# Kernel tuning notes

Measured on AMD Instinct MI355X. Metric: run time of the kernel, lower is better.

## Reference

```python
import jax, jax.numpy as jnp
import numpy as np

ALPHA = 0.1       # args.alpha
T = 1.0           # args.T temperature
SIGMA = 64.0      # Gaussian kernel bandwidth of kernel_function
B_CONST = 1.0     # B in get_lambda
N_ITERS = 50      # 2^-50 << tol=1e-8, matches the break condition of the 1000-iter loop
HW = 256          # image resolution (upsample target)


def _features(feat):
    # get_feature: bilinear upsample (align_corners=False == half-pixel, as jax.image.resize) then sigmoid(x/T)
    n, c, _, _ = feat.shape
    up = jax.image.resize(feat, (n, c, HW, HW), method='bilinear')
    return jax.nn.sigmoid(up / T)


def setup_inputs() -> dict:
    key = jax.random.key(0)
    k1, k2, k3, k4 = jax.random.split(key, 4)
    return {
        'cal_feat': jax.random.normal(k1, (256, 1, 64, 64), jnp.float32),
        'test_feat': jax.random.normal(k2, (32, 1, 64, 64), jnp.float32),
        'cal_gt': jax.random.randint(k3, (256, 1, 256, 256), 0, 2, jnp.int32),
        'test_gt': jax.random.randint(k4, (32, 1, 256, 256), 0, 2, jnp.int32),
    }


def reference(cal_feat, test_feat, cal_gt, test_gt):
    cal_res = _features(cal_feat)    # [N,1,H,W] in (0,1)
    test_res = _features(test_feat)  # [B,1,H,W]
    N = cal_res.shape[0]
    B = test_res.shape[0]
    f32 = cal_res.dtype

    # kernel_function.get_weight: Gaussian RBF on flattened features, plus self-weight 1, row-normalized -> [B, N+1]
    cf = cal_res.reshape(N, -1)
    tf = test_res.reshape(B, -1)
    d2 = (tf * tf).sum(-1)[:, None] + (cf * cf).sum(-1)[None, :] - 2.0 * (tf @ cf.T)
    k = jnp.exp(-d2 / (2.0 * SIGMA * SIGMA))
    w = jnp.concatenate([k, jnp.ones((B, 1), f32)], axis=1)
    w = w / w.sum(axis=1, keepdims=True)

    # FNR_i(t) = #{positive pixels of cal sample i with score < t} / #positives
    # (pred = res >= t, so false negatives are positive pixels with res < t). Precompute sorted
    # positive-pixel scores per cal sample so the bisection is a batched searchsorted.
    gt = (cal_gt > 0).reshape(N, -1)
    pos = jnp.sum(gt, axis=1)                                    # [N]
    scores = jnp.where(gt, cal_res.reshape(N, -1), jnp.inf)
    sorted_scores = jnp.sort(scores, axis=1)                     # [N, HW*HW], padding at +inf
    pos_f = jnp.maximum(pos, 1).astype(f32)

    def fnr_at(t):  # t: [B] thresholds -> [N, B]
        cnt = jax.vmap(lambda s: jnp.searchsorted(s, t, side='left'))(sorted_scores)
        return cnt.astype(f32) / pos_f[:, None]

    # batched bisection on lambda (get_lambda, vectorized over the B test samples)
    def body(carry, _):
        low, high = carry
        lam = 0.5 * (low + high)
        fnr = fnr_at(1.0 - lam)                                   # [N, B]
        risk = jnp.einsum('bn,nb->b', w[:, :-1], fnr) + w[:, -1] * B_CONST
        high = jnp.where(risk < ALPHA, lam, high)
        low = jnp.where(risk >= ALPHA, lam, low)
        return (low, high), None

    init = (jnp.zeros((B,), f32), jnp.ones((B,), f32))
    (low, _), _ = jax.lax.scan(body, init, None, length=N_ITERS)
    lam = low  # _lambda = low after the loop

    # prediction set, size and per-test FNR (get_fnr_list on the test sample)
    pred = test_res >= (1.0 - lam)[:, None, None, None]           # [B,1,H,W] bool
    size = jnp.sum(pred, axis=(1, 2, 3)).astype(f32)
    tgt = test_gt > 0
    tp = jnp.sum(pred & tgt, axis=(1, 2, 3)).astype(f32)
    tpos = jnp.maximum(jnp.sum(tgt, axis=(1, 2, 3)), 1).astype(f32)
    fnr_test = 1.0 - tp / tpos                                    # fdr_tensor, [B]
    return fnr_test, lam, size
```

## Files before the change

kernel.cpp:

```cpp
#include <hip/hip_runtime.h>


#define NPIX 65536
#define HB 16256
#define CDF_STRIDE 16272
#define ALPHA 0.1f
#define STAGE_CAP 35840

#define OFF_TESTRES  0
#define OFF_CALBF    8388608u
#define OFF_TESTBF   41943040u
#define OFF_GROUPED  46137344u
#define OFF_CDF      79691776u
#define OFF_GPART    88023040u
#define OFF_CC       90120192u
#define OFF_THR      90121216u
#define OFF_LAM      90121344u
#define OFF_FACC     90121472u
#define OFF_CDFT     90122240u

typedef __attribute__((ext_vector_type(8))) short bf16x8;
typedef __attribute__((ext_vector_type(16))) float f32x16;

__device__ __forceinline__ unsigned short f2bf_rne(float f) {
  unsigned u = __float_as_uint(f);
  return (unsigned short)((u + 0x7FFFu + ((u >> 16) & 1u)) >> 16);
}

__device__ __forceinline__ int SW(int w) { return w ^ ((w >> 5) & 31); }

__device__ __forceinline__ float sig_v(float a, float b, float wy) {
  float v = a * (1.f - wy) + b * wy;
  return 1.f / (1.f + __expf(-v));
}

__global__ __launch_bounds__(1024, 2) void k_calt(const float* __restrict__ featc,
                                                  const int* __restrict__ gt,
                                                  unsigned short* __restrict__ calbf,
                                                  unsigned short* __restrict__ cdf,
                                                  unsigned short* __restrict__ grouped,
                                                  float* __restrict__ cc,
                                                  const float* __restrict__ featt,
                                                  float* __restrict__ tres,
                                                  unsigned short* __restrict__ tbf) {
  __shared__ unsigned smem[17313];
  __shared__ float sfeat[4096];
  __shared__ __align__(16) unsigned short sstage[STAGE_CAP];
  float* tfeat = (float*)sstage;
  unsigned* gmask = (unsigned*)(sstage + 8192);
  const int tid = threadIdx.x;
  const int lane = tid & 63, wv = tid >> 6;
  const int x = tid & 255, yq = tid >> 8;
  float sx = 0.25f * (float)x - 0.375f;
  int x0 = (int)floorf(sx);
  float wx = sx - (float)x0;
  int x1 = x0 + 1;
  if (x0 < 0) x0 = 0;
  if (x1 > 63) x1 = 63;

  const int n = blockIdx.x;
  const int b = n >> 3, sl = n & 7;
  for (int i = tid; i < HB; i += 1024) smem[i] = 0;
  for (int i = tid; i < 4096; i += 1024) {
    sfeat[i] = featc[n * 4096 + i];
    tfeat[i] = featt[b * 4096 + i];
  }
  {
    const int4* gt4 = (const int4*)(gt + (size_t)n * NPIX);
    for (int w = tid; w < 2048; w += 1024) {
      unsigned m = 0;
      #pragma unroll
      for (int j = 0; j < 8; ++j) {
        int4 g = gt4[w * 8 + j];
        m |= (g.x > 0 ? 1u : 0u) << (j * 4);
        m |= (g.y > 0 ? 2u : 0u) << (j * 4);
        m |= (g.z > 0 ? 4u : 0u) << (j * 4);
        m |= (g.w > 0 ? 8u : 0u) << (j * 4);
      }
      gmask[w] = m;
    }
  }
  unsigned short* cbn = calbf + (size_t)n * NPIX;
  __syncthreads();

  {
    const float* tf0 = tfeat + x0;
    const float* tf1 = tfeat + x1;
    float* resb = tres + (size_t)b * NPIX;
    unsigned short* tbn = tbf + (size_t)b * NPIX;
    const int mt0 = sl * 8 + yq * 2;
    int rp = mt0 - 1 < 0 ? 0 : mt0 - 1;
    float hp = tf0[rp * 64] * (1.f - wx) + tf1[rp * 64] * wx;
    float hc = tf0[mt0 * 64] * (1.f - wx) + tf1[mt0 * 64] * wx;
    #pragma unroll
    for (int q = 0; q < 2; ++q) {
      int m = mt0 + q;
      int rn = m + 1 > 63 ? 63 : m + 1;
      float hn = tf0[rn * 64] * (1.f - wx) + tf1[rn * 64] * wx;
      #pragma unroll
      for (int j = 0; j < 4; ++j) {
        int y = 4 * m + j;
        float sy = 0.25f * (float)y - 0.375f;
        int y0 = (int)floorf(sy);
        float wy = sy - (float)y0;
        float s = sig_v(j < 2 ? hp : hc, j < 2 ? hc : hn, wy);
        int p = (y << 8) + x;
        resb[p] = s;
        tbn[p] = f2bf_rne(s);
      }
      hp = hc; hc = hn;
    }
  }

  const float* f0 = sfeat + x0;
  const float* f1 = sfeat + x1;
  const int m0 = yq * 16;
  unsigned long long pm = 0ull;
  float sumsq = 0.f;
  {
    int rp = m0 - 1 < 0 ? 0 : m0 - 1;
    float hp = f0[rp * 64] * (1.f - wx) + f1[rp * 64] * wx;
    float hc = f0[m0 * 64] * (1.f - wx) + f1[m0 * 64] * wx;
    #pragma unroll 4
    for (int q = 0; q < 16; ++q) {
      int m = m0 + q;
      int rn = m + 1 > 63 ? 63 : m + 1;
      float hn = f0[rn * 64] * (1.f - wx) + f1[rn * 64] * wx;
      #pragma unroll
      for (int j = 0; j < 4; ++j) {
        int y = 4 * m + j;
        float sy = 0.25f * (float)y - 0.375f;
        int y0 = (int)floorf(sy);
        float wy = sy - (float)y0;
        float s = sig_v(j < 2 ? hp : hc, j < 2 ? hc : hn, wy);
        int p = (y << 8) + x;
        unsigned short bh = f2bf_rne(s);
        cbn[p] = bh;
        float sr = __uint_as_float((unsigned)bh << 16);
        sumsq += sr * sr;
        if ((gmask[p >> 5] >> (x & 31)) & 1u) {
          pm |= (1ull << (q * 4 + j));
          atomicAdd(&smem[SW((int)(__float_as_uint(s) >> 16))], 1u);
        }
      }
      hp = hc; hc = hn;
    }
  }
  #pragma unroll
  for (int off = 32; off; off >>= 1) sumsq += __shfl_xor(sumsq, off);
  if (lane == 0) smem[16272 + wv] = __float_as_uint(sumsq);
  __syncthreads();
  if (tid == 0) {
    float c = 0.f;
    for (int w = 0; w < 16; ++w) c += __uint_as_float(smem[16272 + w]);
    cc[n] = c;
  }
  const int base = tid * 16;
  unsigned psum = 0;
  if (tid < 1016) {
    #pragma unroll
    for (int j = 0; j < 16; ++j) psum += smem[SW(base + j)];
  }
  unsigned inc = psum;
  #pragma unroll
  for (int off = 1; off < 64; off <<= 1) {
    unsigned v = __shfl_up(inc, off);
    if (lane >= off) inc += v;
  }
  if (lane == 63) smem[16256 + wv] = inc;
  smem[16288 + tid] = inc - psum;
  __syncthreads();
  {
    unsigned woff = 0;
    for (int w = 0; w < wv; ++w) woff += smem[16256 + w];
    unsigned run = woff + smem[16288 + tid];
    if (tid < 1016) {
      #pragma unroll
      for (int j = 0; j < 16; ++j) {
        int si = SW(base + j);
        unsigned h = smem[si];
        smem[si] = run;
        run += h;
      }
    }
    if (tid == 1015) smem[17312] = run;
  }
  __syncthreads();
  unsigned short* cdfn = cdf + (size_t)n * CDF_STRIDE;
  for (int i = tid; i < HB; i += 1024) cdfn[i] = (unsigned short)smem[SW(i)];
  const unsigned pos = smem[17312];
  if (tid == 0) cdfn[HB] = (unsigned short)pos;
  __syncthreads();
  unsigned short* gn = grouped + (size_t)n * NPIX;
  {
    int rp = m0 - 1 < 0 ? 0 : m0 - 1;
    float hp = f0[rp * 64] * (1.f - wx) + f1[rp * 64] * wx;
    float hc = f0[m0 * 64] * (1.f - wx) + f1[m0 * 64] * wx;
    for (int q = 0; q < 16; ++q) {
      int m = m0 + q;
      int rn = m + 1 > 63 ? 63 : m + 1;
      float hn = f0[rn * 64] * (1.f - wx) + f1[rn * 64] * wx;
      unsigned nib = (unsigned)(pm >> (q * 4)) & 0xFu;
      if (nib) {
        #pragma unroll
        for (int j = 0; j < 4; ++j) {
          if (nib & (1u << j)) {
            int y = 4 * m + j;
            float sy = 0.25f * (float)y - 0.375f;
            int y0 = (int)floorf(sy);
            float wy = sy - (float)y0;
            float s = sig_v(j < 2 ? hp : hc, j < 2 ? hc : hn, wy);
            unsigned bits = __float_as_uint(s);
            unsigned idx = atomicAdd(&smem[SW((int)(bits >> 16))], 1u);
            unsigned short lo = (unsigned short)(bits & 0xFFFFu);
            if (idx < STAGE_CAP) sstage[idx] = lo;
            else gn[idx] = lo;
          }
        }
      }
      hp = hc; hc = hn;
    }
  }
  __syncthreads();
  unsigned lim = pos < STAGE_CAP ? pos : STAGE_CAP;
  for (unsigned i = tid; i < lim; i += 1024) gn[i] = sstage[i];
}

__global__ __launch_bounds__(256) void k_tr(const unsigned short* __restrict__ cdf,
                                            unsigned short* __restrict__ cdfT) {
  __shared__ unsigned short tile[256][136];
  const int b0 = blockIdx.x * 128;
  const int tid = threadIdx.x;
  const unsigned short* src = cdf + (size_t)tid * CDF_STRIDE + b0;
  #pragma unroll
  for (int j = 0; j < 128; j += 8)
    *(int4*)&tile[tid][j] = *(const int4*)(src + j);
  __syncthreads();
  for (int j = 0; j < 128; ++j)
    cdfT[(size_t)(b0 + j) * 256 + tid] = tile[tid][j];
}

__global__ __launch_bounds__(256) void k_gemm(const unsigned short* __restrict__ tbf,
                                              const unsigned short* __restrict__ cbf,
                                              float* __restrict__ gpart) {
  __shared__ __align__(16) unsigned short As[16384];
  __shared__ __align__(16) unsigned short Bs[16384];
  __shared__ float lred[4][1024];
  const int tid = threadIdx.x;
  const int lane = tid & 63, wv = tid >> 6;
  const int r = lane & 31, half = lane >> 5;
  const int nt = blockIdx.x;
  f32x16 acc;
  #pragma unroll
  for (int i = 0; i < 16; ++i) acc[i] = 0.f;
  for (int ch = 0; ch < 2; ++ch) {
    const size_t kbase = (size_t)blockIdx.y * 1024 + ch * 512;
    __syncthreads();
    #pragma unroll
    for (int s = 0; s < 16; ++s) {
      int flat = s * 256 + tid;
      int rem = flat & 2047;
      int row = rem >> 6, kb = rem & 63;
      const unsigned short* src = (flat >= 2048)
          ? cbf + (size_t)(nt * 32 + row) * NPIX + kbase + kb * 8
          : tbf + (size_t)row * NPIX + kbase + kb * 8;
      int slot = ((kb << 5) + row) ^ (kb & 31);
      int4 v = *(const int4*)src;
      *(int4*)((flat >= 2048 ? Bs : As) + slot * 8) = v;
    }
    __syncthreads();
    #pragma unroll
    for (int i = 0; i < 8; ++i) {
      int k8 = (wv << 4) + i * 2 + half;
      int slot = ((k8 << 5) + r) ^ (k8 & 31);
      bf16x8 a = *(const bf16x8*)(As + slot * 8);
      bf16x8 b = *(const bf16x8*)(Bs + slot * 8);
      acc = __builtin_amdgcn_mfma_f32_32x32x16_bf16(a, b, acc, 0, 0, 0);
    }
  }
  #pragma unroll
  for (int rg = 0; rg < 16; ++rg) {
    int m = (rg & 3) + 8 * (rg >> 2) + 4 * half;
    lred[wv][m * 32 + r] = acc[rg];
  }
  __syncthreads();
  float* gp = gpart + (size_t)(blockIdx.y * 8 + nt) * 1024;
  for (int e = tid; e < 1024; e += 256)
    gp[e] = lred[0][e] + lred[1][e] + lred[2][e] + lred[3][e];
}

__global__ __launch_bounds__(512) void k_quantw(const float* __restrict__ gpart,
                                                const float* __restrict__ cc,
                                                const unsigned short* __restrict__ tbf,
                                                const unsigned short* __restrict__ cdf,
                                                const unsigned short* __restrict__ cdfT,
                                                const unsigned short* __restrict__ grouped,
                                                float* __restrict__ lam,
                                                float* __restrict__ thr,
                                                int* __restrict__ facc) {
  __shared__ float qs[256];
  __shared__ float bins[4096];
  __shared__ float red[8];
  __shared__ float tpart[16];
  __shared__ float bc[3];
  __shared__ unsigned sBin;
  const int b = blockIdx.x, tid = threadIdx.x;
  const int lane = tid & 63, wv = tid >> 6;

  if (tid < 4) facc[b * 4 + tid] = 0;
  for (int i = tid; i < 4096; i += 512) bins[i] = 0.f;
  if (tid == 0) sBin = 0xFFFFFFFFu;

  {
    const unsigned short* tbn = tbf + (size_t)b * NPIX;
    const int xa = tid & 255, ya = tid >> 8;
    const int yb = ya + 2;
    float sa = 0.f, sb = 0.f;
    #pragma unroll 4
    for (int it = 0; it < 64; ++it) {
      float ra = __uint_as_float((unsigned)tbn[((it * 4 + ya) << 8) + xa] << 16);
      float rb = __uint_as_float((unsigned)tbn[((it * 4 + yb) << 8) + xa] << 16);
      sa += ra * ra;
      sb += rb * rb;
    }
    #pragma unroll
    for (int off = 32; off; off >>= 1) {
      sa += __shfl_xor(sa, off);
      sb += __shfl_xor(sb, off);
    }
    if (lane == 0) { tpart[wv] = sa; tpart[8 + wv] = sb; }
  }
  __syncthreads();
  if (tid == 0) {
    float t = 0.f;
    for (int w = 0; w < 16; ++w) t += tpart[w];
    bc[2] = t;
  }
  float g = 0.f;
  if (tid < 256) {
    const float* gp = gpart + ((tid >> 5) * 1024) + (b * 32) + (tid & 31);
    #pragma unroll 8
    for (int ks = 0; ks < 64; ++ks) g += gp[(size_t)ks * 8192];
  }
  __syncthreads();
  float k = 0.f;
  if (tid < 256) {
    float d2 = bc[2] + cc[tid] - 2.f * g;
    k = expf(-d2 * (1.f / 8192.f));
  }
  float v = k;
  #pragma unroll
  for (int off = 32; off; off >>= 1) v += __shfl_xor(v, off);
  if (lane == 0) red[wv] = v;
  __syncthreads();
  if (tid == 0) {
    float ws = 1.f;
    for (int w = 0; w < 8; ++w) ws += red[w];
    bc[0] = ws;
  }
  __syncthreads();
  const float wsum = bc[0];
  const float wlast = 1.f / wsum;
  const float R = ALPHA - wlast;
  if (R <= 0.f) {
    if (tid == 0) { lam[b] = 1.0f; thr[b] = 0.0f; }
    return;
  }
  if (tid < 256) {
    unsigned pos = cdf[(size_t)tid * CDF_STRIDE + HB];
    qs[tid] = k / (wsum * (float)(pos ? pos : 1u));
  }
  __syncthreads();

  int lo = 0, hi = HB;
  float baseS = 0.f;
  for (int it = 0; it < 14; ++it) {
    int mid = (lo + hi) >> 1;
    float p = 0.f;
    if (tid < 256) p = qs[tid] * (float)cdfT[(size_t)mid * 256 + tid];
    float r = p;
    #pragma unroll
    for (int off = 32; off; off >>= 1) r += __shfl_xor(r, off);
    if (lane == 0) red[wv] = r;
    __syncthreads();
    if (tid == 0) {
      float s = 0.f;
      for (int w = 0; w < 8; ++w) s += red[w];
      bc[1] = s;
    }
    __syncthreads();
    float S = bc[1];
    if (S < R) { lo = mid; baseS = S; } else { hi = mid; }
  }
  const int B = lo;

  {
    const int n = tid >> 1;
    const float q = qs[n];
    const unsigned short* cn = cdf + (size_t)n * CDF_STRIDE;
    const unsigned short* gn = grouped + (size_t)n * NPIX;
    unsigned e0 = cn[B + 1];
    for (unsigned j = (unsigned)cn[B] + (tid & 1); j < e0; j += 2)
      atomicAdd(&bins[gn[j] >> 4], q);
  }
  __syncthreads();

  if (wv == 0) {
    float s = 0.f;
    for (int j = 0; j < 64; ++j) s += bins[lane * 64 + j];
    float inc = s;
    #pragma unroll
    for (int off = 1; off < 64; off <<= 1) {
      float u = __shfl_up(inc, off);
      if (lane >= off) inc += u;
    }
    float pre = inc - s;
    bool hit = (baseS + pre < R) && (baseS + inc >= R);
    unsigned long long m = __ballot(hit);
    int ow = m ? (__ffsll((unsigned long long)m) - 1) : -1;
    if (lane == ow) {
      float run = baseS + pre;
      unsigned bin = (unsigned)lane * 64 + 63;
      for (int j = 0; j < 64; ++j) {
        float bv = bins[lane * 64 + j];
        if (run + bv >= R) { bin = (unsigned)lane * 64 + j; break; }
        run += bv;
      }
      sBin = bin;
    }
    if (m == 0 && lane == 0) sBin = 4095u;
  }
  __syncthreads();
  if (tid == 0) {
    unsigned tb = ((unsigned)B << 16) | (sBin << 4);
    lam[b] = 1.0f - __uint_as_float(tb | 0x8u);
    thr[b] = __uint_as_float((tb | 0xFu) + 1u);
  }
}

__global__ __launch_bounds__(256) void k_finalp(const float* __restrict__ tres,
                                                const int* __restrict__ tgt,
                                                const float* __restrict__ thr,
                                                const float* __restrict__ lam,
                                                int* __restrict__ facc,
                                                float* __restrict__ out) {
  __shared__ int red[12];
  const int b = blockIdx.x, seg = blockIdx.y, tid = threadIdx.x;
  const int lane = tid & 63, wv = tid >> 6;
  const float th = thr[b];
  const float4* rb4 = (const float4*)(tres + (size_t)b * NPIX + seg * 8192);
  const int4* gb4 = (const int4*)(tgt + (size_t)b * NPIX + seg * 8192);
  int sz = 0, tp = 0, tpos = 0;
  #pragma unroll
  for (int i = 0; i < 8; ++i) {
    float4 r4 = rb4[i * 256 + tid];
    int4 g4 = gb4[i * 256 + tid];
    int p0 = (r4.x >= th), t0 = (g4.x > 0);
    int p1 = (r4.y >= th), t1 = (g4.y > 0);
    int p2 = (r4.z >= th), t2 = (g4.z > 0);
    int p3 = (r4.w >= th), t3 = (g4.w > 0);
    sz += p0 + p1 + p2 + p3;
    tp += (p0 & t0) + (p1 & t1) + (p2 & t2) + (p3 & t3);
    tpos += t0 + t1 + t2 + t3;
  }
  #pragma unroll
  for (int off = 32; off; off >>= 1) {
    sz += __shfl_xor(sz, off);
    tp += __shfl_xor(tp, off);
    tpos += __shfl_xor(tpos, off);
  }
  if (lane == 0) { red[wv] = sz; red[4 + wv] = tp; red[8 + wv] = tpos; }
  __syncthreads();
  if (tid == 0) {
    int s0 = red[0] + red[1] + red[2] + red[3];
    int s1 = red[4] + red[5] + red[6] + red[7];
    int s2 = red[8] + red[9] + red[10] + red[11];
    atomicAdd(&facc[b * 4 + 0], s0);
    atomicAdd(&facc[b * 4 + 1], s1);
    atomicAdd(&facc[b * 4 + 2], s2);
    __threadfence();
    int done = atomicAdd(&facc[b * 4 + 3], 1);
    if (done == 7) {
      int f0 = atomicAdd(&facc[b * 4 + 0], 0);
      int f1 = atomicAdd(&facc[b * 4 + 1], 0);
      int f2 = atomicAdd(&facc[b * 4 + 2], 0);
      float tposf = (float)(f2 > 0 ? f2 : 1);
      out[b] = 1.f - (float)f1 / tposf;
      out[32 + b] = lam[b];
      out[64 + b] = (float)f0;
    }
  }
}

extern "C" void kernel_launch(void* const* d_in, const int* in_sizes, int n_in,
                              void* d_out, int out_size, void* d_ws, size_t ws_size,
                              hipStream_t stream) {
  const float* cal_feat = (const float*)d_in[0];
  const float* test_feat = (const float*)d_in[1];
  const int* cal_gt = (const int*)d_in[2];
  const int* test_gt = (const int*)d_in[3];
  float* out = (float*)d_out;
  char* ws = (char*)d_ws;

  float* test_res = (float*)(ws + OFF_TESTRES);
  unsigned short* cal_bf = (unsigned short*)(ws + OFF_CALBF);
  unsigned short* test_bf = (unsigned short*)(ws + OFF_TESTBF);
  unsigned short* grouped = (unsigned short*)(ws + OFF_GROUPED);
  unsigned short* cdf = (unsigned short*)(ws + OFF_CDF);
  unsigned short* cdfT = (unsigned short*)(ws + OFF_CDFT);
  float* gpart = (float*)(ws + OFF_GPART);
  float* cc = (float*)(ws + OFF_CC);
  float* thr = (float*)(ws + OFF_THR);
  float* lam = (float*)(ws + OFF_LAM);
  int* facc = (int*)(ws + OFF_FACC);

  k_calt<<<dim3(256), dim3(1024), 0, stream>>>(cal_feat, cal_gt, cal_bf, cdf, grouped, cc,
                                               test_feat, test_res, test_bf);
  k_tr<<<dim3(127), dim3(256), 0, stream>>>(cdf, cdfT);
  k_gemm<<<dim3(8, 64), dim3(256), 0, stream>>>(test_bf, cal_bf, gpart);
  k_quantw<<<dim3(32), dim3(512), 0, stream>>>(gpart, cc, test_bf, cdf, cdfT, grouped,
                                               lam, thr, facc);
  k_finalp<<<dim3(32, 8), dim3(256), 0, stream>>>(test_res, test_gt, thr, lam, facc, out);
}
```

Measured before the change: 223.9 us.

## Vectorize upsample to 4 pixels per thread and fuse cdf transpose into GEMM

The upsample/sigmoid in k_calt now has each thread produce four horizontally adjacent pixels. Neighbouring feature columns are shared across the four outputs, and the bf16 and float stores become vectorized uint2 and float4 writes. The separate cdf transpose kernel is folded into the GEMM launch as an extra grid row of blocks, which removes one kernel launch and lets the transpose overlap with the GEMM. The trade-off is higher register pressure per thread in k_calt and a different pixel-to-thread mapping for the shared-memory histogram atomics. The LDS buffer is also unified for both roles.

```diff
diff --git a/kernel.cpp b/kernel.cpp
--- a/kernel.cpp
+++ b/kernel.cpp
@@ -22,9 +22,9 @@
 typedef __attribute__((ext_vector_type(8))) short bf16x8;
 typedef __attribute__((ext_vector_type(16))) float f32x16;
 
-__device__ __forceinline__ unsigned short f2bf_rne(float f) {
+__device__ __forceinline__ unsigned f2bf_rne(float f) {
   unsigned u = __float_as_uint(f);
-  return (unsigned short)((u + 0x7FFFu + ((u >> 16) & 1u)) >> 16);
+  return (u + 0x7FFFu + ((u >> 16) & 1u)) >> 16;
 }
 
 __device__ __forceinline__ int SW(int w) { return w ^ ((w >> 5) & 31); }
@@ -33,6 +33,17 @@
   float v = a * (1.f - wy) + b * wy;
   return 1.f / (1.f + __expf(-v));
 }
+
+#define ROWH(F, r, h0, h1, h2, h3)                                        \
+  {                                                                       \
+    float fL_ = (F)[(r) * 64 + cL];                                       \
+    float fM_ = (F)[(r) * 64 + cM];                                       \
+    float fR_ = (F)[(r) * 64 + cR];                                       \
+    h0 = fL_ * (1.f - wx0) + fM_ * wx0;                                   \
+    h1 = fL_ * (1.f - wx1) + fM_ * wx1;                                   \
+    h2 = fM_ * (1.f - wx2) + fR_ * wx2;                                   \
+    h3 = fM_ * (1.f - wx3) + fR_ * wx3;                                   \
+  }
 
 __global__ __launch_bounds__(1024, 2) void k_calt(const float* __restrict__ featc,
                                                   const int* __restrict__ gt,
@@ -50,13 +61,21 @@
   unsigned* gmask = (unsigned*)(sstage + 8192);
   const int tid = threadIdx.x;
   const int lane = tid & 63, wv = tid >> 6;
-  const int x = tid & 255, yq = tid >> 8;
-  float sx = 0.25f * (float)x - 0.375f;
-  int x0 = (int)floorf(sx);
-  float wx = sx - (float)x0;
-  int x1 = x0 + 1;
-  if (x0 < 0) x0 = 0;
-  if (x1 > 63) x1 = 63;
+  const int xg = tid & 63, band = tid >> 6;
+  float wx0, wx1, wx2, wx3;
+  {
+    float sx0 = 0.25f * (float)(4 * xg + 0) - 0.375f;
+    float sx1 = 0.25f * (float)(4 * xg + 1) - 0.375f;
+    float sx2 = 0.25f * (float)(4 * xg + 2) - 0.375f;
+    float sx3 = 0.25f * (float)(4 * xg + 3) - 0.375f;
+    wx0 = sx0 - (float)((int)floorf(sx0));
+    wx1 = sx1 - (float)((int)floorf(sx1));
+    wx2 = sx2 - (float)((int)floorf(sx2));
+    wx3 = sx3 - (float)((int)floorf(sx3));
+  }
+  const int cL = (xg == 0) ? 0 : xg - 1;
+  const int cM = xg;
+  const int cR = (xg == 63) ? 63 : xg + 1;
 
   const int n = blockIdx.x;
   const int b = n >> 3, sl = n & 7;
@@ -84,66 +103,94 @@
   __syncthreads();
 
   {
-    const float* tf0 = tfeat + x0;
-    const float* tf1 = tfeat + x1;
+    const int tr0 = sl * 32 + 2 * band;
+    const int mt = tr0 >> 2, j0 = tr0 & 3;
+    float tp0, tp1, tp2, tp3, tc0, tc1, tc2, tc3, tn0, tn1, tn2, tn3;
+    int rp = (mt == 0) ? 0 : mt - 1;
+    int rn = (mt == 63) ? 63 : mt + 1;
+    ROWH(tfeat, rp, tp0, tp1, tp2, tp3);
+    ROWH(tfeat, mt, tc0, tc1, tc2, tc3);
+    ROWH(tfeat, rn, tn0, tn1, tn2, tn3);
     float* resb = tres + (size_t)b * NPIX;
     unsigned short* tbn = tbf + (size_t)b * NPIX;
-    const int mt0 = sl * 8 + yq * 2;
-    int rp = mt0 - 1 < 0 ? 0 : mt0 - 1;
-    float hp = tf0[rp * 64] * (1.f - wx) + tf1[rp * 64] * wx;
-    float hc = tf0[mt0 * 64] * (1.f - wx) + tf1[mt0 * 64] * wx;
-    #pragma unroll
-    for (int q = 0; q < 2; ++q) {
-      int m = mt0 + q;
-      int rn = m + 1 > 63 ? 63 : m + 1;
-      float hn = tf0[rn * 64] * (1.f - wx) + tf1[rn * 64] * wx;
+    #pragma unroll
+    for (int jj = 0; jj < 2; ++jj) {
+      int j = j0 + jj;
+      int y = 4 * mt + j;
+      float sy = 0.25f * (float)y - 0.375f;
+      int y0i = (int)floorf(sy);
+      float wy = sy - (float)y0i;
+      float a0 = j < 2 ? tp0 : tc0, b0 = j < 2 ? tc0 : tn0;
+      float a1 = j < 2 ? tp1 : tc1, b1 = j < 2 ? tc1 : tn1;
+      float a2 = j < 2 ? tp2 : tc2, b2 = j < 2 ? tc2 : tn2;
+      float a3 = j < 2 ? tp3 : tc3, b3 = j < 2 ? tc3 : tn3;
+      float s0 = sig_v(a0, b0, wy), s1 = sig_v(a1, b1, wy);
+      float s2 = sig_v(a2, b2, wy), s3 = sig_v(a3, b3, wy);
+      float4 rv = {s0, s1, s2, s3};
+      *(float4*)(resb + (y << 8) + 4 * xg) = rv;
+      uint2 pk;
+      pk.x = f2bf_rne(s0) | (f2bf_rne(s1) << 16);
+      pk.y = f2bf_rne(s2) | (f2bf_rne(s3) << 16);
+      *(uint2*)(tbn + (y << 8) + 4 * xg) = pk;
+    }
+  }
+
+  const int mq0 = band * 4;
+  unsigned long long pm = 0ull;
+  float sumsq = 0.f;
+  {
+    float hp0, hp1, hp2, hp3, hc0, hc1, hc2, hc3, hn0, hn1, hn2, hn3;
+    int rp = (mq0 == 0) ? 0 : mq0 - 1;
+    ROWH(sfeat, rp, hp0, hp1, hp2, hp3);
+    ROWH(sfeat, mq0, hc0, hc1, hc2, hc3);
+    for (int qq = 0; qq < 4; ++qq) {
+      int m = mq0 + qq;
+      int rn = (m == 63) ? 63 : m + 1;
+      ROWH(sfeat, rn, hn0, hn1, hn2, hn3);
       #pragma unroll
       for (int j = 0; j < 4; ++j) {
         int y = 4 * m + j;
         float sy = 0.25f * (float)y - 0.375f;
-        int y0 = (int)floorf(sy);
-        float wy = sy - (float)y0;
-        float s = sig_v(j < 2 ? hp : hc, j < 2 ? hc : hn, wy);
-        int p = (y << 8) + x;
-        resb[p] = s;
-        tbn[p] = f2bf_rne(s);
-      }
-      hp = hc; hc = hn;
-    }
-  }
-
-  const float* f0 = sfeat + x0;
-  const float* f1 = sfeat + x1;
-  const int m0 = yq * 16;
-  unsigned long long pm = 0ull;
-  float sumsq = 0.f;
-  {
-    int rp = m0 - 1 < 0 ? 0 : m0 - 1;
-    float hp = f0[rp * 64] * (1.f - wx) + f1[rp * 64] * wx;
-    float hc = f0[m0 * 64] * (1.f - wx) + f1[m0 * 64] * wx;
-    #pragma unroll 4
-    for (int q = 0; q < 16; ++q) {
-      int m = m0 + q;
-      int rn = m + 1 > 63 ? 63 : m + 1;
-      float hn = f0[rn * 64] * (1.f - wx) + f1[rn * 64] * wx;
-      #pragma unroll
-      for (int j = 0; j < 4; ++j) {
-        int y = 4 * m + j;
-        float sy = 0.25f * (float)y - 0.375f;
-        int y0 = (int)floorf(sy);
-        float wy = sy - (float)y0;
-        float s = sig_v(j < 2 ? hp : hc, j < 2 ? hc : hn, wy);
-        int p = (y << 8) + x;
-        unsigned short bh = f2bf_rne(s);
-        cbn[p] = bh;
-        float sr = __uint_as_float((unsigned)bh << 16);
-        sumsq += sr * sr;
-        if ((gmask[p >> 5] >> (x & 31)) & 1u) {
-          pm |= (1ull << (q * 4 + j));
-          atomicAdd(&smem[SW((int)(__float_as_uint(s) >> 16))], 1u);
+        int y0i = (int)floorf(sy);
+        float wy = sy - (float)y0i;
+        float a0 = j < 2 ? hp0 : hc0, b0 = j < 2 ? hc0 : hn0;
+        float a1 = j < 2 ? hp1 : hc1, b1 = j < 2 ? hc1 : hn1;
+        float a2 = j < 2 ? hp2 : hc2, b2 = j < 2 ? hc2 : hn2;
+        float a3 = j < 2 ? hp3 : hc3, b3 = j < 2 ? hc3 : hn3;
+        float s0 = sig_v(a0, b0, wy), s1 = sig_v(a1, b1, wy);
+        float s2 = sig_v(a2, b2, wy), s3 = sig_v(a3, b3, wy);
+        unsigned u0 = f2bf_rne(s0), u1 = f2bf_rne(s1);
+        unsigned u2 = f2bf_rne(s2), u3 = f2bf_rne(s3);
+        uint2 pk;
+        pk.x = u0 | (u1 << 16);
+        pk.y = u2 | (u3 << 16);
+        *(uint2*)(cbn + (y << 8) + 4 * xg) = pk;
+        float r0 = __uint_as_float(u0 << 16), r1 = __uint_as_float(u1 << 16);
+        float r2 = __uint_as_float(u2 << 16), r3 = __uint_as_float(u3 << 16);
+        sumsq += r0 * r0;
+        sumsq += r1 * r1;
+        sumsq += r2 * r2;
+        sumsq += r3 * r3;
+        unsigned nib = (gmask[(y << 3) + (xg >> 3)] >> (4 * (xg & 7))) & 0xFu;
+        if (nib & 1u) {
+          pm |= 1ull << (qq * 16 + j * 4 + 0);
+          atomicAdd(&smem[SW((int)(__float_as_uint(s0) >> 16))], 1u);
+        }
+        if (nib & 2u) {
+          pm |= 1ull << (qq * 16 + j * 4 + 1);
+          atomicAdd(&smem[SW((int)(__float_as_uint(s1) >> 16))], 1u);
+        }
+        if (nib & 4u) {
+          pm |= 1ull << (qq * 16 + j * 4 + 2);
+          atomicAdd(&smem[SW((int)(__float_as_uint(s2) >> 16))], 1u);
+        }
+        if (nib & 8u) {
+          pm |= 1ull << (qq * 16 + j * 4 + 3);
+          atomicAdd(&smem[SW((int)(__float_as_uint(s3) >> 16))], 1u);
         }
       }
-      hp = hc; hc = hn;
+      hp0 = hc0; hp1 = hc1; hp2 = hc2; hp3 = hc3;
+      hc0 = hn0; hc1 = hn1; hc2 = hn2; hc3 = hn3;
     }
   }
   #pragma unroll
@@ -193,32 +240,47 @@
   __syncthreads();
   unsigned short* gn = grouped + (size_t)n * NPIX;
   {
-    int rp = m0 - 1 < 0 ? 0 : m0 - 1;
-    float hp = f0[rp * 64] * (1.f - wx) + f1[rp * 64] * wx;
-    float hc = f0[m0 * 64] * (1.f - wx) + f1[m0 * 64] * wx;
-    for (int q = 0; q < 16; ++q) {
-      int m = m0 + q;
-      int rn = m + 1 > 63 ? 63 : m + 1;
-      float hn = f0[rn * 64] * (1.f - wx) + f1[rn * 64] * wx;
-      unsigned nib = (unsigned)(pm >> (q * 4)) & 0xFu;
-      if (nib) {
+    float hp0, hp1, hp2, hp3, hc0, hc1, hc2, hc3, hn0, hn1, hn2, hn3;
+    int rp = (mq0 == 0) ? 0 : mq0 - 1;
+    ROWH(sfeat, rp, hp0, hp1, hp2, hp3);
+    ROWH(sfeat, mq0, hc0, hc1, hc2, hc3);
+    for (int qq = 0; qq < 4; ++qq) {
+      int m = mq0 + qq;
+      int rn = (m == 63) ? 63 : m + 1;
+      ROWH(sfeat, rn, hn0, hn1, hn2, hn3);
+      unsigned qb = (unsigned)(pm >> (qq * 16)) & 0xFFFFu;
+      if (qb) {
         #pragma unroll
         for (int j = 0; j < 4; ++j) {
-          if (nib & (1u << j)) {
+          unsigned nib = (qb >> (j * 4)) & 0xFu;
+          if (nib) {
             int y = 4 * m + j;
             float sy = 0.25f * (float)y - 0.375f;
-            int y0 = (int)floorf(sy);
-            float wy = sy - (float)y0;
-            float s = sig_v(j < 2 ? hp : hc, j < 2 ? hc : hn, wy);
-            unsigned bits = __float_as_uint(s);
-            unsigned idx = atomicAdd(&smem[SW((int)(bits >> 16))], 1u);
-            unsigned short lo = (unsigned short)(bits & 0xFFFFu);
-            if (idx < STAGE_CAP) sstage[idx] = lo;
-            else gn[idx] = lo;
+            int y0i = (int)floorf(sy);
+            float wy = sy - (float)y0i;
+            float a0 = j < 2 ? hp0 : hc0, b0 = j < 2 ? hc0 : hn0;
+            float a1 = j < 2 ? hp1 : hc1, b1 = j < 2 ? hc1 : hn1;
+            float a2 = j < 2 ? hp2 : hc2, b2 = j < 2 ? hc2 : hn2;
+            float a3 = j < 2 ? hp3 : hc3, b3 = j < 2 ? hc3 : hn3;
+            #pragma unroll
+            for (int k = 0; k < 4; ++k) {
+              if (nib & (1u << k)) {
+                float s = k == 0 ? sig_v(a0, b0, wy)
+                        : k == 1 ? sig_v(a1, b1, wy)
+                        : k == 2 ? sig_v(a2, b2, wy)
+                                 : sig_v(a3, b3, wy);
+                unsigned bits = __float_as_uint(s);
+                unsigned idx = atomicAdd(&smem[SW((int)(bits >> 16))], 1u);
+                unsigned short lo = (unsigned short)(bits & 0xFFFFu);
+                if (idx < STAGE_CAP) sstage[idx] = lo;
+                else gn[idx] = lo;
+              }
+            }
           }
         }
       }
-      hp = hc; hc = hn;
+      hp0 = hc0; hp1 = hc1; hp2 = hc2; hp3 = hc3;
+      hc0 = hn0; hc1 = hn1; hc2 = hn2; hc3 = hn3;
     }
   }
   __syncthreads();
@@ -226,27 +288,31 @@
   for (unsigned i = tid; i < lim; i += 1024) gn[i] = sstage[i];
 }
 
-__global__ __launch_bounds__(256) void k_tr(const unsigned short* __restrict__ cdf,
-                                            unsigned short* __restrict__ cdfT) {
-  __shared__ unsigned short tile[256][136];
-  const int b0 = blockIdx.x * 128;
+__global__ __launch_bounds__(256) void k_gemmtr(const unsigned short* __restrict__ tbf,
+                                                const unsigned short* __restrict__ cbf,
+                                                float* __restrict__ gpart,
+                                                const unsigned short* __restrict__ cdf,
+                                                unsigned short* __restrict__ cdfT) {
+  __shared__ __align__(16) char lds[81920];
   const int tid = threadIdx.x;
-  const unsigned short* src = cdf + (size_t)tid * CDF_STRIDE + b0;
-  #pragma unroll
-  for (int j = 0; j < 128; j += 8)
-    *(int4*)&tile[tid][j] = *(const int4*)(src + j);
-  __syncthreads();
-  for (int j = 0; j < 128; ++j)
-    cdfT[(size_t)(b0 + j) * 256 + tid] = tile[tid][j];
-}
-
-__global__ __launch_bounds__(256) void k_gemm(const unsigned short* __restrict__ tbf,
-                                              const unsigned short* __restrict__ cbf,
-                                              float* __restrict__ gpart) {
-  __shared__ __align__(16) unsigned short As[16384];
-  __shared__ __align__(16) unsigned short Bs[16384];
-  __shared__ float lred[4][1024];
-  const int tid = threadIdx.x;
+  if (blockIdx.y == 64) {
+    unsigned short (*tile)[136] = (unsigned short (*)[136])lds;
+    for (int t = blockIdx.x; t < 127; t += 8) {
+      const int b0 = t * 128;
+      const unsigned short* src = cdf + (size_t)tid * CDF_STRIDE + b0;
+      __syncthreads();
+      #pragma unroll
+      for (int j = 0; j < 128; j += 8)
+        *(int4*)&tile[tid][j] = *(const int4*)(src + j);
+      __syncthreads();
+      for (int j = 0; j < 128; ++j)
+        cdfT[(size_t)(b0 + j) * 256 + tid] = tile[tid][j];
+    }
+    return;
+  }
+  unsigned short* As = (unsigned short*)lds;
+  unsigned short* Bs = (unsigned short*)(lds + 32768);
+  float (*lred)[1024] = (float (*)[1024])(lds + 65536);
   const int lane = tid & 63, wv = tid >> 6;
   const int r = lane & 31, half = lane >> 5;
   const int nt = blockIdx.x;
@@ -516,8 +582,7 @@
 
   k_calt<<<dim3(256), dim3(1024), 0, stream>>>(cal_feat, cal_gt, cal_bf, cdf, grouped, cc,
                                                test_feat, test_res, test_bf);
-  k_tr<<<dim3(127), dim3(256), 0, stream>>>(cdf, cdfT);
-  k_gemm<<<dim3(8, 64), dim3(256), 0, stream>>>(test_bf, cal_bf, gpart);
+  k_gemmtr<<<dim3(8, 65), dim3(256), 0, stream>>>(test_bf, cal_bf, gpart, cdf, cdfT);
   k_quantw<<<dim3(32), dim3(512), 0, stream>>>(gpart, cc, test_bf, cdf, cdfT, grouped,
                                                lam, thr, facc);
   k_finalp<<<dim3(32, 8), dim3(256), 0, stream>>>(test_res, test_gt, thr, lam, facc, out);
```

Measured after the change: 273.2 us. 1.22x slower.
